# Performance work log

Measured on AMD Instinct MI355X. Metric: run time of the kernel, lower is better.

Reference implementation:

```python
import jax, jax.numpy as jnp
import numpy as np


def setup_inputs() -> dict:
    key = jax.random.key(0)
    inputs = jax.random.normal(key, (4096, 8192), dtype=jnp.float32)
    return {"inputs": inputs, "k": 512}


def reference(inputs, k):
    # Original: kth_smallest = sort_ascending(inputs)[..., n-1-k]
    # i.e. the (k+1)-th largest value per row. Equivalent via top_k.
    # Keep only elements STRICTLY greater than that threshold.
    thresh = jax.lax.top_k(inputs, k + 1)[0][..., -1]  # [batch]
    mask = (inputs > thresh[:, None]).astype(inputs.dtype)
    return inputs * mask
```

## Files before the change

kernel.cpp:

```cpp
#include <hip/hip_runtime.h>
#include <stdint.h>


constexpr int COLS = 8192;
constexpr int TPB  = 256;
constexpr int EPT  = COLS / TPB;
constexpr int VPT  = EPT / 4;
constexpr int NBIN = 2048;
constexpr int NREP = 2;

__device__ __forceinline__ uint32_t map_f32(uint32_t u) {
  return (u & 0x80000000u) ? ~u : (u | 0x80000000u);
}
__device__ __forceinline__ float unmap_f32(uint32_t m) {
  return __uint_as_float((m & 0x80000000u) ? (m ^ 0x80000000u) : ~m);
}

__global__ __launch_bounds__(TPB)
void ksparse_kernel(const float* __restrict__ in, const int* __restrict__ kptr,
                    float* __restrict__ out) {
  __shared__ __align__(16) uint32_t hist[NREP * NBIN];
  __shared__ uint32_t wtot[4];
  __shared__ int s_dmax;
  __shared__ uint32_t s_above;

  const int t    = threadIdx.x;
  const int wave = t >> 6;
  const int lane = t & 63;
  const size_t rowbase = (size_t)blockIdx.x * COLS;

  uint32_t m[EPT];
  const float4* inp = (const float4*)(in + rowbase);
#pragma unroll
  for (int i = 0; i < VPT; ++i) {
    float4 v = inp[t + i * TPB];
    m[4 * i + 0] = map_f32(__float_as_uint(v.x));
    m[4 * i + 1] = map_f32(__float_as_uint(v.y));
    m[4 * i + 2] = map_f32(__float_as_uint(v.z));
    m[4 * i + 3] = map_f32(__float_as_uint(v.w));
  }

  uint32_t kk = (uint32_t)(*kptr) + 1u;
  uint32_t pref = 0;

  const int shifts[3]  = {21, 10, 0};
  const int dmask[3]   = {0x7FF, 0x7FF, 0x3FF};
  const int cshifts[3] = {0, 21, 10};

#pragma unroll 1
  for (int pass = 0; pass < 3; ++pass) {
    const int shift = shifts[pass];
    const uint32_t dm = (uint32_t)dmask[pass];

    uint4* h4 = (uint4*)hist;
#pragma unroll
    for (int i = 0; i < (NREP * NBIN / 4) / TPB; ++i)
      h4[t + i * TPB] = make_uint4(0u, 0u, 0u, 0u);
    if (t == 0) s_dmax = -1;
    __syncthreads();

    uint32_t* h = &hist[(wave >> 1) * NBIN];
    if (pass == 0) {
#pragma unroll
      for (int i = 0; i < EPT; ++i)
        atomicAdd(&h[m[i] >> 21], 1u);
    } else {
      const int cs = cshifts[pass];
#pragma unroll
      for (int i = 0; i < EPT; ++i) {
        if ((m[i] >> cs) == pref)
          atomicAdd(&h[(m[i] >> shift) & dm], 1u);
      }
    }
    __syncthreads();

    const uint4* hv = (const uint4*)hist;
    uint4 a0 = hv[2 * t];
    uint4 a1 = hv[2 * t + 1];
    uint4 b0 = hv[NBIN / 4 + 2 * t];
    uint4 b1 = hv[NBIN / 4 + 2 * t + 1];
    uint32_t c0 = a0.x + b0.x, c1 = a0.y + b0.y, c2 = a0.z + b0.z, c3 = a0.w + b0.w;
    uint32_t c4 = a1.x + b1.x, c5 = a1.y + b1.y, c6 = a1.z + b1.z, c7 = a1.w + b1.w;
    uint32_t sl[8];
    sl[7] = c7;       sl[6] = sl[7] + c6; sl[5] = sl[6] + c5; sl[4] = sl[5] + c4;
    sl[3] = sl[4] + c3; sl[2] = sl[3] + c2; sl[1] = sl[2] + c1; sl[0] = sl[1] + c0;
    const uint32_t total = sl[0];

    uint32_t s = total;
#pragma unroll
    for (int off = 1; off < 64; off <<= 1) {
      uint32_t tmp = __shfl_down(s, off, 64);
      s += (lane + off < 64) ? tmp : 0u;
    }
    if (lane == 0) wtot[wave] = s;
    __syncthreads();

    uint32_t hi = 0;
#pragma unroll
    for (int w = 1; w < 4; ++w)
      if (w > wave) hi += wtot[w];
    const uint32_t excl = hi + (s - total);

    int best = -1;
#pragma unroll
    for (int j = 7; j >= 0; --j) {
      if (best < 0 && excl + sl[j] >= kk) best = j;
    }
    if (best >= 0) atomicMax(&s_dmax, t * 8 + best);
    __syncthreads();

    const int d = s_dmax;
    if (t == (d >> 3)) {
      const int j = d & 7;
      s_above = excl + ((j < 7) ? sl[j + 1] : 0u);
    }
    __syncthreads();

    kk -= s_above;
    pref = (pass == 0) ? (uint32_t)d
                       : ((pref << ((pass == 2) ? 10 : 11)) | (uint32_t)d);
    __syncthreads();
  }

  const uint32_t T = pref;

  float4* op = (float4*)(out + rowbase);
#pragma unroll
  for (int i = 0; i < VPT; ++i) {
    float4 v;
    uint32_t mm;
    mm  = m[4 * i + 0]; v.x = (mm > T) ? unmap_f32(mm) : 0.0f;
    mm  = m[4 * i + 1]; v.y = (mm > T) ? unmap_f32(mm) : 0.0f;
    mm  = m[4 * i + 2]; v.z = (mm > T) ? unmap_f32(mm) : 0.0f;
    mm  = m[4 * i + 3]; v.w = (mm > T) ? unmap_f32(mm) : 0.0f;
    op[t + i * TPB] = v;
  }
}

extern "C" void kernel_launch(void* const* d_in, const int* in_sizes, int n_in,
                              void* d_out, int out_size, void* d_ws, size_t ws_size,
                              hipStream_t stream) {
  const float* in  = (const float*)d_in[0];
  const int*   k   = (const int*)d_in[1];
  float*       out = (float*)d_out;
  int rows = in_sizes[0] / COLS;
  if (rows < 1) rows = 1;
  ksparse_kernel<<<rows, TPB, 0, stream>>>(in, k, out);
}
```

Before: 240.1 us.

## Compact top-bucket candidates to shared memory and refine threshold with small radix passes

After the first 11-bit histogram pass, elements in the selected bucket are compacted into a shared-memory candidate list. Three 7-bit radix passes with 128-bin histograms then run over that list instead of re-scanning all 32 register elements per thread. The first histogram is also fused into the load loop, and the bucket index and count-above are packed into one atomicMax. The candidate list is capped at 2048 entries, so a row whose selected bucket holds more elements than that would give a wrong threshold.

```diff
diff --git a/kernel.cpp b/kernel.cpp
--- a/kernel.cpp
+++ b/kernel.cpp
@@ -2,12 +2,12 @@
 #include <stdint.h>
 
 
-constexpr int COLS = 8192;
-constexpr int TPB  = 256;
-constexpr int EPT  = COLS / TPB;
-constexpr int VPT  = EPT / 4;
-constexpr int NBIN = 2048;
-constexpr int NREP = 2;
+constexpr int COLS  = 8192;
+constexpr int TPB   = 256;
+constexpr int EPT   = COLS / TPB;
+constexpr int VPT   = EPT / 4;
+constexpr int NBIN0 = 2048;
+constexpr int CAP   = 2048;
 
 __device__ __forceinline__ uint32_t map_f32(uint32_t u) {
   return (u & 0x80000000u) ? ~u : (u | 0x80000000u);
@@ -19,70 +19,55 @@
 __global__ __launch_bounds__(TPB)
 void ksparse_kernel(const float* __restrict__ in, const int* __restrict__ kptr,
                     float* __restrict__ out) {
-  __shared__ __align__(16) uint32_t hist[NREP * NBIN];
+  __shared__ __align__(16) uint32_t hist[2 * NBIN0];
+  __shared__ uint32_t th[3 * 128];
   __shared__ uint32_t wtot[4];
-  __shared__ int s_dmax;
-  __shared__ uint32_t s_above;
+  __shared__ uint32_t s_packed;
+  __shared__ uint32_t s_cnt;
+  __shared__ uint32_t s_sel[3];
 
   const int t    = threadIdx.x;
   const int wave = t >> 6;
   const int lane = t & 63;
   const size_t rowbase = (size_t)blockIdx.x * COLS;
 
+  const float4* inp = (const float4*)(in + rowbase);
+  float4 v[VPT];
+#pragma unroll
+  for (int i = 0; i < VPT; ++i) v[i] = inp[t + i * TPB];
+
+  uint4* h4 = (uint4*)hist;
+#pragma unroll
+  for (int i = 0; i < 4; ++i) h4[t + i * TPB] = make_uint4(0u, 0u, 0u, 0u);
+  th[t] = 0u;
+  if (t < 128) th[256 + t] = 0u;
+  if (t == 0) { s_packed = 0u; s_cnt = 0u; }
+  uint32_t kk = (uint32_t)(*kptr) + 1u;
+  __syncthreads();
+
   uint32_t m[EPT];
-  const float4* inp = (const float4*)(in + rowbase);
+  uint32_t* h = &hist[(wave >> 1) * NBIN0];
 #pragma unroll
   for (int i = 0; i < VPT; ++i) {
-    float4 v = inp[t + i * TPB];
-    m[4 * i + 0] = map_f32(__float_as_uint(v.x));
-    m[4 * i + 1] = map_f32(__float_as_uint(v.y));
-    m[4 * i + 2] = map_f32(__float_as_uint(v.z));
-    m[4 * i + 3] = map_f32(__float_as_uint(v.w));
+    m[4 * i + 0] = map_f32(__float_as_uint(v[i].x));
+    m[4 * i + 1] = map_f32(__float_as_uint(v[i].y));
+    m[4 * i + 2] = map_f32(__float_as_uint(v[i].z));
+    m[4 * i + 3] = map_f32(__float_as_uint(v[i].w));
+    atomicAdd(&h[m[4 * i + 0] >> 21], 1u);
+    atomicAdd(&h[m[4 * i + 1] >> 21], 1u);
+    atomicAdd(&h[m[4 * i + 2] >> 21], 1u);
+    atomicAdd(&h[m[4 * i + 3] >> 21], 1u);
   }
+  __syncthreads();
 
-  uint32_t kk = (uint32_t)(*kptr) + 1u;
-  uint32_t pref = 0;
-
-  const int shifts[3]  = {21, 10, 0};
-  const int dmask[3]   = {0x7FF, 0x7FF, 0x3FF};
-  const int cshifts[3] = {0, 21, 10};
-
-#pragma unroll 1
-  for (int pass = 0; pass < 3; ++pass) {
-    const int shift = shifts[pass];
-    const uint32_t dm = (uint32_t)dmask[pass];
-
-    uint4* h4 = (uint4*)hist;
-#pragma unroll
-    for (int i = 0; i < (NREP * NBIN / 4) / TPB; ++i)
-      h4[t + i * TPB] = make_uint4(0u, 0u, 0u, 0u);
-    if (t == 0) s_dmax = -1;
-    __syncthreads();
-
-    uint32_t* h = &hist[(wave >> 1) * NBIN];
-    if (pass == 0) {
-#pragma unroll
-      for (int i = 0; i < EPT; ++i)
-        atomicAdd(&h[m[i] >> 21], 1u);
-    } else {
-      const int cs = cshifts[pass];
-#pragma unroll
-      for (int i = 0; i < EPT; ++i) {
-        if ((m[i] >> cs) == pref)
-          atomicAdd(&h[(m[i] >> shift) & dm], 1u);
-      }
-    }
-    __syncthreads();
-
+  {
     const uint4* hv = (const uint4*)hist;
-    uint4 a0 = hv[2 * t];
-    uint4 a1 = hv[2 * t + 1];
-    uint4 b0 = hv[NBIN / 4 + 2 * t];
-    uint4 b1 = hv[NBIN / 4 + 2 * t + 1];
+    uint4 a0 = hv[2 * t], a1 = hv[2 * t + 1];
+    uint4 b0 = hv[512 + 2 * t], b1 = hv[512 + 2 * t + 1];
     uint32_t c0 = a0.x + b0.x, c1 = a0.y + b0.y, c2 = a0.z + b0.z, c3 = a0.w + b0.w;
     uint32_t c4 = a1.x + b1.x, c5 = a1.y + b1.y, c6 = a1.z + b1.z, c7 = a1.w + b1.w;
     uint32_t sl[8];
-    sl[7] = c7;       sl[6] = sl[7] + c6; sl[5] = sl[6] + c5; sl[4] = sl[5] + c4;
+    sl[7] = c7;         sl[6] = sl[7] + c6; sl[5] = sl[6] + c5; sl[4] = sl[5] + c4;
     sl[3] = sl[4] + c3; sl[2] = sl[3] + c2; sl[1] = sl[2] + c1; sl[0] = sl[1] + c0;
     const uint32_t total = sl[0];
 
@@ -103,37 +88,90 @@
 
     int best = -1;
 #pragma unroll
-    for (int j = 7; j >= 0; --j) {
+    for (int j = 7; j >= 0; --j)
       if (best < 0 && excl + sl[j] >= kk) best = j;
+    if (best >= 0) {
+      const uint32_t above = excl + ((best < 7) ? sl[best + 1] : 0u);
+      atomicMax(&s_packed, ((uint32_t)(t * 8 + best) << 14) | above);
     }
-    if (best >= 0) atomicMax(&s_dmax, t * 8 + best);
-    __syncthreads();
+  }
+  __syncthreads();
 
-    const int d = s_dmax;
-    if (t == (d >> 3)) {
-      const int j = d & 7;
-      s_above = excl + ((j < 7) ? sl[j + 1] : 0u);
+  const uint32_t pk = s_packed;
+  const uint32_t d0 = pk >> 14;
+  kk -= (pk & 0x3FFFu);
+
+  uint32_t* cand = &hist[NBIN0];
+#pragma unroll
+  for (int i = 0; i < EPT; ++i) {
+    if ((m[i] >> 21) == d0) {
+      uint32_t idx = atomicAdd(&s_cnt, 1u);
+      if (idx < CAP) cand[idx] = m[i] & 0x1FFFFFu;
+    }
+  }
+  __syncthreads();
+  const uint32_t Cc = (s_cnt < (uint32_t)CAP) ? s_cnt : (uint32_t)CAP;
+
+  uint32_t tpref = 0;
+#pragma unroll 1
+  for (int j = 0; j < 3; ++j) {
+    const int dsh = 14 - 7 * j;
+    uint32_t* thj = &th[j * 128];
+    for (uint32_t idx = t; idx < Cc; idx += TPB) {
+      const uint32_t c = cand[idx];
+      const bool ok = (j == 0) || ((c >> (dsh + 7)) == tpref);
+      if (ok) atomicAdd(&thj[(c >> dsh) & 127u], 1u);
     }
     __syncthreads();
 
-    kk -= s_above;
-    pref = (pass == 0) ? (uint32_t)d
-                       : ((pref << ((pass == 2) ? 10 : 11)) | (uint32_t)d);
+    if (wave == 0) {
+      uint32_t a = thj[lane], b = thj[64 + lane];
+      uint32_t sb = b, sa = a;
+#pragma unroll
+      for (int off = 1; off < 64; off <<= 1) {
+        uint32_t t1 = __shfl_down(sb, off, 64);
+        uint32_t t2 = __shfl_down(sa, off, 64);
+        const bool inr = (lane + off < 64);
+        sb += inr ? t1 : 0u;
+        sa += inr ? t2 : 0u;
+      }
+      const uint32_t tb = __shfl(sb, 0, 64);
+      sa += tb;
+      const unsigned long long mb = __ballot(sb >= kk);
+      uint32_t d, ab;
+      if (mb) {
+        const int hb = 63 - __builtin_clzll(mb);
+        const uint32_t nx = __shfl(sb, (hb + 1) & 63, 64);
+        d = 64 + hb;
+        ab = (hb == 63) ? 0u : nx;
+      } else {
+        const unsigned long long ma = __ballot(sa >= kk);
+        const int ha = 63 - __builtin_clzll(ma);
+        const uint32_t nx = __shfl(sa, (ha + 1) & 63, 64);
+        d = (uint32_t)ha;
+        ab = (ha == 63) ? tb : nx;
+      }
+      if (lane == 0) s_sel[j] = (d << 16) | ab;
+    }
     __syncthreads();
+
+    const uint32_t sel = s_sel[j];
+    tpref = (tpref << 7) | (sel >> 16);
+    kk -= (sel & 0xFFFFu);
   }
 
-  const uint32_t T = pref;
+  const uint32_t T = (d0 << 21) | tpref;
 
   float4* op = (float4*)(out + rowbase);
 #pragma unroll
   for (int i = 0; i < VPT; ++i) {
-    float4 v;
+    float4 w;
     uint32_t mm;
-    mm  = m[4 * i + 0]; v.x = (mm > T) ? unmap_f32(mm) : 0.0f;
-    mm  = m[4 * i + 1]; v.y = (mm > T) ? unmap_f32(mm) : 0.0f;
-    mm  = m[4 * i + 2]; v.z = (mm > T) ? unmap_f32(mm) : 0.0f;
-    mm  = m[4 * i + 3]; v.w = (mm > T) ? unmap_f32(mm) : 0.0f;
-    op[t + i * TPB] = v;
+    mm = m[4 * i + 0]; w.x = (mm > T) ? unmap_f32(mm) : 0.0f;
+    mm = m[4 * i + 1]; w.y = (mm > T) ? unmap_f32(mm) : 0.0f;
+    mm = m[4 * i + 2]; w.z = (mm > T) ? unmap_f32(mm) : 0.0f;
+    mm = m[4 * i + 3]; w.w = (mm > T) ? unmap_f32(mm) : 0.0f;
+    op[t + i * TPB] = w;
   }
 }
 
```

Measured after the change: 235.1 us. 1.02x faster.
